# Performance work log

Hardware: AMD Instinct MI355X
Metric: run time of the kernel (lower is better)

The kernel has to match this reference:

```python
import jax, jax.numpy as jnp
import numpy as np

N = 50000
T = 6
E = 800000
F_IN = 64
HID = 64
HEADS = 4
NEG_SLOPE = 0.2
BN_EPS = 1e-5


def _gat_layer(x, src, dst, W, att_src, att_dst, bias, concat):
    # x: [N, Fin]; W: [Fin, H*C]; att_*: [H, C]; src/dst: [E+N] (self loops appended)
    n = x.shape[0]
    H, C = att_src.shape
    xl = (x @ W).reshape(n, H, C)                     # [N, H, C]
    a_src = jnp.sum(xl * att_src[None], axis=-1)      # [N, H]
    a_dst = jnp.sum(xl * att_dst[None], axis=-1)      # [N, H]
    e = jax.nn.leaky_relu(a_src[src] + a_dst[dst], NEG_SLOPE)  # [E', H]
    # segment softmax over destination nodes (every node has a self loop)
    m = jax.ops.segment_max(e, dst, num_segments=n)
    ex = jnp.exp(e - m[dst])
    s = jax.ops.segment_sum(ex, dst, num_segments=n)
    alpha = ex / (s[dst] + 1e-16)                     # [E', H]
    msg = alpha[:, :, None] * xl[src]                 # [E', H, C]
    out = jax.ops.segment_sum(msg, dst, num_segments=n)  # [N, H, C]
    if concat:
        out = out.reshape(n, H * C)
    else:
        out = out.mean(axis=1)
    return out + bias


def _forward(x_seq, edge_index, W1, as1, ad1, b1, W2, as2, ad2, b2,
             cw1, cb1, g1, be1, cw2, cb2, g2, be2, lw1, lb1, lw2, lb2):
    n = x_seq.shape[1]
    self_loop = jnp.arange(n, dtype=edge_index.dtype)
    src = jnp.concatenate([edge_index[0], self_loop])
    dst = jnp.concatenate([edge_index[1], self_loop])

    def per_t(x):
        h = _gat_layer(x, src, dst, W1, as1, ad1, b1, concat=True)
        h = jax.nn.elu(h)
        h = _gat_layer(h, src, dst, W2, as2, ad2, b2, concat=False)
        h = jax.nn.elu(h)
        return h                                      # [N, HID]

    temporal = jax.vmap(per_t)(x_seq)                 # [T, N, HID]
    temporal = jnp.transpose(temporal, (1, 2, 0))     # [N, HID, T]

    def conv_bn_relu(t, cw, cb, g, be):
        y = jax.lax.conv_general_dilated(
            t, cw, window_strides=(1,), padding=[(1, 1)],
            dimension_numbers=('NCH', 'OIH', 'NCH')) + cb[None, :, None]
        # BatchNorm1d in eval mode, running_mean=0, running_var=1
        y = y * (g / jnp.sqrt(1.0 + BN_EPS))[None, :, None] + be[None, :, None]
        return jax.nn.relu(y)

    t = conv_bn_relu(temporal, cw1, cb1, g1, be1)
    t = conv_bn_relu(t, cw2, cb2, g2, be2)
    pooled = t.mean(axis=-1)                          # adaptive avg pool -> [N, HID]
    h = jax.nn.relu(pooled @ lw1 + lb1)
    logits = h @ lw2 + lb2                            # [N, 1]
    return logits


def setup_inputs() -> dict:
    key = jax.random.key(0)
    ks = jax.random.split(key, 20)
    C1 = HID // HEADS  # 16
    s = 0.1
    return {
        'x_seq': jax.random.normal(ks[0], (T, N, F_IN), jnp.float32),
        'edge_index': jax.random.randint(ks[1], (2, E), 0, N, jnp.int32),
        'W1': jax.random.normal(ks[2], (F_IN, HEADS * C1), jnp.float32) * s,
        'as1': jax.random.normal(ks[3], (HEADS, C1), jnp.float32) * s,
        'ad1': jax.random.normal(ks[4], (HEADS, C1), jnp.float32) * s,
        'b1': jnp.zeros((HEADS * C1,), jnp.float32),
        'W2': jax.random.normal(ks[5], (HID, HEADS * HID), jnp.float32) * s,
        'as2': jax.random.normal(ks[6], (HEADS, HID), jnp.float32) * s,
        'ad2': jax.random.normal(ks[7], (HEADS, HID), jnp.float32) * s,
        'b2': jnp.zeros((HID,), jnp.float32),
        'cw1': jax.random.normal(ks[8], (HID, HID, 3), jnp.float32) * s,
        'cb1': jnp.zeros((HID,), jnp.float32),
        'g1': jnp.ones((HID,), jnp.float32),
        'be1': jnp.zeros((HID,), jnp.float32),
        'cw2': jax.random.normal(ks[9], (HID, HID, 3), jnp.float32) * s,
        'cb2': jnp.zeros((HID,), jnp.float32),
        'g2': jnp.ones((HID,), jnp.float32),
        'be2': jnp.zeros((HID,), jnp.float32),
        'lw1': jax.random.normal(ks[10], (HID, HID // 2), jnp.float32) * s,
        'lb1': jnp.zeros((HID // 2,), jnp.float32),
        'lw2': jax.random.normal(ks[11], (HID // 2, 1), jnp.float32) * s,
        'lb2': jnp.zeros((1,), jnp.float32),
    }


def reference(x_seq, edge_index, W1, as1, ad1, b1, W2, as2, ad2, b2,
              cw1, cb1, g1, be1, cw2, cb2, g2, be2, lw1, lb1, lw2, lb2):
    return _forward(x_seq, edge_index, W1, as1, ad1, b1, W2, as2, ad2, b2,
                    cw1, cb1, g1, be1, cw2, cb2, g2, be2, lw1, lb1, lw2, lb2)
```

## Files before the change

### kernel.cpp

```cpp
#include <hip/hip_runtime.h>
#include <math.h>

#define NN 50000
#define EE 800000
#define TT 6

__device__ __forceinline__ float lrelu(float x){ return x > 0.f ? x : 0.2f*x; }
__device__ __forceinline__ float eluf(float x){ return x > 0.f ? x : expm1f(x); }

__global__ void k_init_counts(int* __restrict__ c){
  int i = blockIdx.x*256 + threadIdx.x;
  if (i < NN) c[i] = 1;
}

__global__ void k_hist(const int* __restrict__ dst, int* __restrict__ c){
  int i = blockIdx.x*256 + threadIdx.x;
  if (i < EE) atomicAdd(&c[dst[i]], 1);
}

__global__ void k_scanA(const int* __restrict__ cnt, int* __restrict__ excl,
                        int* __restrict__ bsum){
  __shared__ int sh[1024];
  int tid = threadIdx.x;
  int i = blockIdx.x*1024 + tid;
  int v = (i < NN) ? cnt[i] : 0;
  int x = v;
  sh[tid] = x; __syncthreads();
  for (int off = 1; off < 1024; off <<= 1){
    int y = (tid >= off) ? sh[tid - off] : 0;
    __syncthreads();
    x += y; sh[tid] = x; __syncthreads();
  }
  if (i < NN) excl[i] = x - v;
  if (tid == 1023) bsum[blockIdx.x] = x;
}

__global__ void k_scanB(int* __restrict__ bsum, int nb){
  if (threadIdx.x == 0){
    int run = 0;
    for (int b = 0; b < nb; ++b){ int t = bsum[b]; bsum[b] = run; run += t; }
  }
}

__global__ void k_scanC(const int* __restrict__ excl, const int* __restrict__ bsum,
                        int* __restrict__ rowptr, int* __restrict__ cursor){
  int i = blockIdx.x*1024 + threadIdx.x;
  if (i < NN){
    int v = excl[i] + bsum[blockIdx.x];
    rowptr[i] = v; cursor[i] = v;
  }
  if (i == 0) rowptr[NN] = EE + NN;
}

__global__ void k_scatter(const int* __restrict__ ei, int* __restrict__ cursor,
                          int* __restrict__ csr){
  int i = blockIdx.x*256 + threadIdx.x;
  if (i < EE){
    int d = ei[EE + i];
    int p = atomicAdd(&cursor[d], 1);
    csr[p] = ei[i];
  } else if (i < EE + NN){
    int v = i - EE;
    int p = atomicAdd(&cursor[v], 1);
    csr[p] = v;
  }
}

__global__ void k_prep(const float* __restrict__ W1, const float* __restrict__ as1,
                       const float* __restrict__ ad1,
                       const float* __restrict__ W2, const float* __restrict__ as2,
                       const float* __restrict__ ad2,
                       const float* __restrict__ cw1, const float* __restrict__ cw2,
                       const float* __restrict__ lw1,
                       float* __restrict__ Was1, float* __restrict__ Wad1,
                       float* __restrict__ Wat2, float* __restrict__ Wb,
                       float4* __restrict__ wq1, float4* __restrict__ wq2,
                       float* __restrict__ lw1t){
  int tid = threadIdx.x;
  int k = tid >> 2, h = tid & 3;
  float s1 = 0.f, d1 = 0.f, s2 = 0.f, d2 = 0.f;
  for (int c = 0; c < 16; ++c){
    float w = W1[k*64 + h*16 + c];
    s1 += w * as1[h*16 + c];
    d1 += w * ad1[h*16 + c];
  }
  for (int c = 0; c < 64; ++c){
    float w = W2[k*256 + h*64 + c];
    s2 += w * as2[h*64 + c];
    d2 += w * ad2[h*64 + c];
  }
  Was1[k*4+h] = s1; Wad1[k*4+h] = d1;
  Wat2[k*8 + h] = s2; Wat2[k*8 + 4 + h] = d2;
  for (int idx = tid; idx < 256*64; idx += 256){
    int kf = idx >> 6, c = idx & 63;
    int hh = kf >> 6, kk = kf & 63;
    Wb[idx] = W2[kk*256 + hh*64 + c];
  }
  for (int idx = tid; idx < 64*64; idx += 256){
    int o = idx >> 6, i = idx & 63;
    wq1[idx] = make_float4(cw1[o*192+i*3], cw1[o*192+i*3+1], cw1[o*192+i*3+2], 0.f);
    wq2[idx] = make_float4(cw2[o*192+i*3], cw2[o*192+i*3+1], cw2[o*192+i*3+2], 0.f);
  }
  for (int idx = tid; idx < 32*64; idx += 256){
    int j = idx >> 6, kk = idx & 63;
    lw1t[idx] = lw1[kk*32 + j];
  }
}

__global__ __launch_bounds__(256) void k_gemm_att1(const float* __restrict__ A,
                            const float* __restrict__ W,
                            const float* __restrict__ Was, const float* __restrict__ Wad,
                            float* __restrict__ Xl, float* __restrict__ a_src,
                            float* __restrict__ a_dst){
  __shared__ float At[64][16];
  int tid = threadIdx.x;
  int r0 = blockIdx.x * 16;
  {
    const float4* A4 = (const float4*)(A + (size_t)r0*64);
    float4 v = A4[tid];
    int r = tid >> 4, k4 = (tid & 15) << 2;
    At[k4+0][r] = v.x; At[k4+1][r] = v.y;
    At[k4+2][r] = v.z; At[k4+3][r] = v.w;
  }
  __syncthreads();
  int col = tid & 63;
  int rbase = (tid >> 6) << 2;
  float acc0=0.f, acc1=0.f, acc2=0.f, acc3=0.f;
  for (int k = 0; k < 64; ++k){
    float w = W[k*64 + col];
    float4 a4 = *(const float4*)&At[k][rbase];
    acc0 += a4.x*w; acc1 += a4.y*w; acc2 += a4.z*w; acc3 += a4.w*w;
  }
  Xl[(size_t)(r0+rbase+0)*64 + col] = acc0;
  Xl[(size_t)(r0+rbase+1)*64 + col] = acc1;
  Xl[(size_t)(r0+rbase+2)*64 + col] = acc2;
  Xl[(size_t)(r0+rbase+3)*64 + col] = acc3;
  if (tid < 128){
    int r = tid >> 3, jx = tid & 7;
    int h = jx & 3;
    const float* Wv = (jx < 4) ? Was : Wad;
    float a = 0.f;
    for (int k = 0; k < 64; ++k) a += At[k][r] * Wv[k*4 + h];
    if (jx < 4) a_src[(r0 + r)*4 + h] = a;
    else        a_dst[(r0 + r)*4 + h] = a;
  }
}

__global__ void k_agg1(const float* __restrict__ xl, const float* __restrict__ a_src,
                       const float* __restrict__ a_dst, const float* __restrict__ b1,
                       const float* __restrict__ Wat2,
                       const int* __restrict__ rowptr, const int* __restrict__ csr,
                       float* __restrict__ h1,
                       float* __restrict__ a_src2, float* __restrict__ a_dst2){
  int lane = threadIdx.x & 63;
  int wid  = threadIdx.x >> 6;
  int n = blockIdx.x*4 + wid;
  int h = lane >> 4;
  float ad = a_dst[n*4 + h];
  int rs = rowptr[n], re = rowptr[n+1];
  float s = 0.f, acc = 0.f;
  int j = rs;
  for (; j + 4 <= re; j += 4){
    int sn0=csr[j], sn1=csr[j+1], sn2=csr[j+2], sn3=csr[j+3];
    float e0=a_src[sn0*4+h], e1=a_src[sn1*4+h], e2=a_src[sn2*4+h], e3=a_src[sn3*4+h];
    float x0=xl[(size_t)sn0*64+lane], x1=xl[(size_t)sn1*64+lane];
    float x2=xl[(size_t)sn2*64+lane], x3=xl[(size_t)sn3*64+lane];
    float p0=__expf(lrelu(e0+ad)), p1=__expf(lrelu(e1+ad));
    float p2=__expf(lrelu(e2+ad)), p3=__expf(lrelu(e3+ad));
    s += p0; acc += p0*x0;
    s += p1; acc += p1*x1;
    s += p2; acc += p2*x2;
    s += p3; acc += p3*x3;
  }
  for (; j < re; ++j){
    int sn = csr[j];
    float p = __expf(lrelu(a_src[sn*4+h] + ad));
    float x = xl[(size_t)sn*64 + lane];
    s += p; acc += p*x;
  }
  float hv = eluf(acc/(s + 1e-16f) + b1[lane]);
  h1[(size_t)n*64 + lane] = hv;
  float4 wA = ((const float4*)Wat2)[lane*2];
  float4 wB = ((const float4*)Wat2)[lane*2 + 1];
  float p[8];
  p[0]=hv*wA.x; p[1]=hv*wA.y; p[2]=hv*wA.z; p[3]=hv*wA.w;
  p[4]=hv*wB.x; p[5]=hv*wB.y; p[6]=hv*wB.z; p[7]=hv*wB.w;
#pragma unroll
  for (int off = 32; off >= 1; off >>= 1){
#pragma unroll
    for (int q = 0; q < 8; ++q) p[q] += __shfl_xor(p[q], off);
  }
  if (lane == 0){
    ((float4*)a_src2)[n] = make_float4(p[0],p[1],p[2],p[3]);
    ((float4*)a_dst2)[n] = make_float4(p[4],p[5],p[6],p[7]);
  }
}

__global__ void k_agg2(const float* __restrict__ h1, const float* __restrict__ a_src,
                       const float* __restrict__ a_dst,
                       const int* __restrict__ rowptr, const int* __restrict__ csr,
                       float* __restrict__ agg){
  int lane = threadIdx.x & 63;
  int wid  = threadIdx.x >> 6;
  int n = blockIdx.x*4 + wid;
  float4 ad = ((const float4*)a_dst)[n];
  int rs = rowptr[n], re = rowptr[n+1];
  float s0=0.f,s1=0.f,s2=0.f,s3=0.f;
  float g0=0.f,g1=0.f,g2=0.f,g3=0.f;
  int j = rs;
  for (; j + 4 <= re; j += 4){
    int sa=csr[j], sb=csr[j+1], sc=csr[j+2], sd=csr[j+3];
    float4 ea = ((const float4*)a_src)[sa];
    float4 eb = ((const float4*)a_src)[sb];
    float4 ec = ((const float4*)a_src)[sc];
    float4 ed = ((const float4*)a_src)[sd];
    float xa = h1[(size_t)sa*64 + lane];
    float xb = h1[(size_t)sb*64 + lane];
    float xc = h1[(size_t)sc*64 + lane];
    float xd = h1[(size_t)sd*64 + lane];
    float pa0=__expf(lrelu(ea.x+ad.x)), pa1=__expf(lrelu(ea.y+ad.y));
    float pa2=__expf(lrelu(ea.z+ad.z)), pa3=__expf(lrelu(ea.w+ad.w));
    float pb0=__expf(lrelu(eb.x+ad.x)), pb1=__expf(lrelu(eb.y+ad.y));
    float pb2=__expf(lrelu(eb.z+ad.z)), pb3=__expf(lrelu(eb.w+ad.w));
    float pc0=__expf(lrelu(ec.x+ad.x)), pc1=__expf(lrelu(ec.y+ad.y));
    float pc2=__expf(lrelu(ec.z+ad.z)), pc3=__expf(lrelu(ec.w+ad.w));
    float pd0=__expf(lrelu(ed.x+ad.x)), pd1=__expf(lrelu(ed.y+ad.y));
    float pd2=__expf(lrelu(ed.z+ad.z)), pd3=__expf(lrelu(ed.w+ad.w));
    s0 += pa0+pb0+pc0+pd0; g0 += pa0*xa + pb0*xb + pc0*xc + pd0*xd;
    s1 += pa1+pb1+pc1+pd1; g1 += pa1*xa + pb1*xb + pc1*xc + pd1*xd;
    s2 += pa2+pb2+pc2+pd2; g2 += pa2*xa + pb2*xb + pc2*xc + pd2*xd;
    s3 += pa3+pb3+pc3+pd3; g3 += pa3*xa + pb3*xb + pc3*xc + pd3*xd;
  }
  for (; j < re; ++j){
    int sn = csr[j];
    float4 ev = ((const float4*)a_src)[sn];
    float x = h1[(size_t)sn*64 + lane];
    float p0=__expf(lrelu(ev.x+ad.x)), p1=__expf(lrelu(ev.y+ad.y));
    float p2=__expf(lrelu(ev.z+ad.z)), p3=__expf(lrelu(ev.w+ad.w));
    s0 += p0; g0 += p0*x;
    s1 += p1; g1 += p1*x;
    s2 += p2; g2 += p2*x;
    s3 += p3; g3 += p3*x;
  }
  size_t base = (size_t)n*256 + lane;
  agg[base      ] = g0/(s0 + 1e-16f);
  agg[base +  64] = g1/(s1 + 1e-16f);
  agg[base + 128] = g2/(s2 + 1e-16f);
  agg[base + 192] = g3/(s3 + 1e-16f);
}

__global__ __launch_bounds__(256) void k_out2(const float* __restrict__ agg,
                                              const float* __restrict__ Wb,
                                              const float* __restrict__ b2,
                                              float* __restrict__ ht){
  __shared__ float AtF[256*20];
  int tid = threadIdx.x;
  int r0 = blockIdx.x * 16;
  const float4* A4 = (const float4*)(agg + (size_t)r0*256);
#pragma unroll
  for (int jj = 0; jj < 4; ++jj){
    int m = tid + 256*jj;
    float4 v = A4[m];
    int row = m >> 6, k0 = (m & 63) << 2;
    AtF[(k0+0)*20 + row] = v.x;
    AtF[(k0+1)*20 + row] = v.y;
    AtF[(k0+2)*20 + row] = v.z;
    AtF[(k0+3)*20 + row] = v.w;
  }
  __syncthreads();
  int col = tid & 63;
  int rbase = (tid >> 6) << 2;
  float acc0=0.f, acc1=0.f, acc2=0.f, acc3=0.f;
  for (int k = 0; k < 256; ++k){
    float w = Wb[(size_t)k*64 + col];
    float4 a4 = *(const float4*)&AtF[k*20 + rbase];
    acc0 += a4.x*w; acc1 += a4.y*w; acc2 += a4.z*w; acc3 += a4.w*w;
  }
  float bb = b2[col];
  ht[(size_t)(r0+rbase+0)*64 + col] = eluf(0.25f*acc0 + bb);
  ht[(size_t)(r0+rbase+1)*64 + col] = eluf(0.25f*acc1 + bb);
  ht[(size_t)(r0+rbase+2)*64 + col] = eluf(0.25f*acc2 + bb);
  ht[(size_t)(r0+rbase+3)*64 + col] = eluf(0.25f*acc3 + bb);
}

__global__ __launch_bounds__(256) void k_xposeQ(const float* __restrict__ htb,
                                                float* __restrict__ Xq){
  __shared__ float T[64][65];
  int tid = threadIdx.x;
  int q = tid >> 6, lane = tid & 63;
  int n0 = blockIdx.x * 64;
  int nw = n0 + lane;
  bool ok = (nw < NN);
  for (int jj = 0; jj < 16; ++jj){
    int ch = q*16 + jj;
    if (ok){
      Xq[((size_t)ch*8 + 0)*NN + nw] = 0.f;
      Xq[((size_t)ch*8 + 7)*NN + nw] = 0.f;
    }
  }
  for (int t = 0; t < 6; ++t){
    for (int jj = 0; jj < 16; ++jj){
      int nn = q*16 + jj;
      int nsrc = n0 + nn; if (nsrc >= NN) nsrc = NN-1;
      T[nn][lane] = htb[((size_t)t*NN + nsrc)*64 + lane];
    }
    __syncthreads();
    if (ok){
      for (int jj = 0; jj < 16; ++jj){
        int ch = q*16 + jj;
        Xq[((size_t)ch*8 + t + 1)*NN + nw] = T[lane][ch];
      }
    }
    __syncthreads();
  }
}

__global__ __launch_bounds__(256) void k_convQ(
    const float* __restrict__ Xq, float* __restrict__ C1,
    const float4* __restrict__ wq1, const float* __restrict__ cb1,
    const float* __restrict__ g1,   const float* __restrict__ be1,
    const float4* __restrict__ wq2, const float* __restrict__ cb2,
    const float* __restrict__ g2,   const float* __restrict__ be2,
    const float* __restrict__ lw1t, const float* __restrict__ lb1,
    const float* __restrict__ lw2,  const float* __restrict__ lb2,
    float* __restrict__ out){
  __shared__ float pool_lds[64][65];
  __shared__ float outp[4][64];
  int lane = threadIdx.x & 63;
  int w = __builtin_amdgcn_readfirstlane(threadIdx.x >> 6);
  int n0 = blockIdx.x * 64;
  int n = n0 + lane;
  int nc = (n < NN) ? n : (NN-1);
  bool ok = (n < NN);

#pragma unroll
  for (int oc = 0; oc < 2; ++oc){
    int ob = w*16 + oc*8;
    float acc[8][6];
#pragma unroll
    for (int o = 0; o < 8; ++o){
      float c = cb1[ob+o];
#pragma unroll
      for (int t = 0; t < 6; ++t) acc[o][t] = c;
    }
    for (int i = 0; i < 64; ++i){
      const float* xp = Xq + (size_t)i*8*NN + nc;
      float x0 = xp[0*NN], x1 = xp[1*NN], x2 = xp[2*NN], x3 = xp[3*NN];
      float x4 = xp[4*NN], x5 = xp[5*NN], x6 = xp[6*NN], x7 = xp[7*NN];
#pragma unroll
      for (int o = 0; o < 8; ++o){
        float4 wv = wq1[(ob+o)*64 + i];
        acc[o][0] += wv.x*x0 + wv.y*x1 + wv.z*x2;
        acc[o][1] += wv.x*x1 + wv.y*x2 + wv.z*x3;
        acc[o][2] += wv.x*x2 + wv.y*x3 + wv.z*x4;
        acc[o][3] += wv.x*x3 + wv.y*x4 + wv.z*x5;
        acc[o][4] += wv.x*x4 + wv.y*x5 + wv.z*x6;
        acc[o][5] += wv.x*x5 + wv.y*x6 + wv.z*x7;
      }
    }
    if (ok){
#pragma unroll
      for (int o = 0; o < 8; ++o){
        float bns = g1[ob+o]*rsqrtf(1.f + 1e-5f), be = be1[ob+o];
        float* cp = C1 + (size_t)(ob+o)*8*NN + n;
        cp[0*NN] = 0.f; cp[7*NN] = 0.f;
#pragma unroll
        for (int t = 0; t < 6; ++t) cp[(t+1)*NN] = fmaxf(acc[o][t]*bns + be, 0.f);
      }
    }
  }
  __syncthreads();
#pragma unroll
  for (int oc = 0; oc < 2; ++oc){
    int ob = w*16 + oc*8;
    float acc[8][6];
#pragma unroll
    for (int o = 0; o < 8; ++o){
      float c = cb2[ob+o];
#pragma unroll
      for (int t = 0; t < 6; ++t) acc[o][t] = c;
    }
    for (int i = 0; i < 64; ++i){
      const float* xp = C1 + (size_t)i*8*NN + nc;
      float x0 = xp[0*NN], x1 = xp[1*NN], x2 = xp[2*NN], x3 = xp[3*NN];
      float x4 = xp[4*NN], x5 = xp[5*NN], x6 = xp[6*NN], x7 = xp[7*NN];
#pragma unroll
      for (int o = 0; o < 8; ++o){
        float4 wv = wq2[(ob+o)*64 + i];
        acc[o][0] += wv.x*x0 + wv.y*x1 + wv.z*x2;
        acc[o][1] += wv.x*x1 + wv.y*x2 + wv.z*x3;
        acc[o][2] += wv.x*x2 + wv.y*x3 + wv.z*x4;
        acc[o][3] += wv.x*x3 + wv.y*x4 + wv.z*x5;
        acc[o][4] += wv.x*x4 + wv.y*x5 + wv.z*x6;
        acc[o][5] += wv.x*x5 + wv.y*x6 + wv.z*x7;
      }
    }
#pragma unroll
    for (int o = 0; o < 8; ++o){
      float bns = g2[ob+o]*rsqrtf(1.f + 1e-5f), be = be2[ob+o];
      float pooled = 0.f;
#pragma unroll
      for (int t = 0; t < 6; ++t) pooled += fmaxf(acc[o][t]*bns + be, 0.f);
      pool_lds[ob+o][lane] = pooled*(1.f/6.f);
    }
  }
  __syncthreads();
  {
    float hacc[8];
#pragma unroll
    for (int jj = 0; jj < 8; ++jj) hacc[jj] = 0.f;
    for (int k = 0; k < 64; ++k){
      float pk = pool_lds[k][lane];
#pragma unroll
      for (int jj = 0; jj < 8; ++jj)
        hacc[jj] += pk * lw1t[(w*8+jj)*64 + k];
    }
    float po = 0.f;
#pragma unroll
    for (int jj = 0; jj < 8; ++jj)
      po += fmaxf(hacc[jj] + lb1[w*8+jj], 0.f) * lw2[w*8+jj];
    outp[w][lane] = po;
  }
  __syncthreads();
  if (w == 0 && ok)
    out[n] = outp[0][lane] + outp[1][lane] + outp[2][lane] + outp[3][lane] + lb2[0];
}

extern "C" void kernel_launch(void* const* d_in, const int* in_sizes, int n_in,
                              void* d_out, int out_size, void* d_ws, size_t ws_size,
                              hipStream_t stream) {
  const float* x_seq = (const float*)d_in[0];
  const int*   ei    = (const int*)  d_in[1];
  const float* W1  = (const float*)d_in[2];
  const float* as1 = (const float*)d_in[3];
  const float* ad1 = (const float*)d_in[4];
  const float* b1  = (const float*)d_in[5];
  const float* W2  = (const float*)d_in[6];
  const float* as2 = (const float*)d_in[7];
  const float* ad2 = (const float*)d_in[8];
  const float* b2  = (const float*)d_in[9];
  const float* cw1 = (const float*)d_in[10];
  const float* cb1 = (const float*)d_in[11];
  const float* g1  = (const float*)d_in[12];
  const float* be1 = (const float*)d_in[13];
  const float* cw2 = (const float*)d_in[14];
  const float* cb2 = (const float*)d_in[15];
  const float* g2  = (const float*)d_in[16];
  const float* be2 = (const float*)d_in[17];
  const float* lw1 = (const float*)d_in[18];
  const float* lb1 = (const float*)d_in[19];
  const float* lw2 = (const float*)d_in[20];
  const float* lb2 = (const float*)d_in[21];
  float* out = (float*)d_out;

  const size_t QSZ = (size_t)64*8*NN*sizeof(float);
  char* wp = (char*)d_ws;
  auto alloc = [&](size_t bytes) -> char* {
    char* p = wp; wp += (bytes + 255) & ~(size_t)255; return p;
  };
  char* region1 = alloc(QSZ);
  float* Was1 = (float*)alloc(256*sizeof(float));
  float* Wad1 = (float*)alloc(256*sizeof(float));
  float* Wat2 = (float*)alloc(64*8*sizeof(float));
  float* Wb   = (float*)alloc(256*64*sizeof(float));
  float4* wq1 = (float4*)alloc(64*64*sizeof(float4));
  float4* wq2 = (float4*)alloc(64*64*sizeof(float4));
  float* lw1t = (float*)alloc(32*64*sizeof(float));
  char* region2 = alloc(QSZ);

  char* sp = region1;
  auto salloc = [&](size_t bytes) -> char* {
    char* p = sp; sp += (bytes + 255) & ~(size_t)255; return p;
  };
  int*   counts = (int*)  salloc(NN*sizeof(int));
  int*   excl   = (int*)  salloc(NN*sizeof(int));
  int*   bsum   = (int*)  salloc(64*sizeof(int));
  int*   rowptr = (int*)  salloc((NN+1)*sizeof(int));
  int*   cursor = (int*)  salloc(NN*sizeof(int));
  int*   csr    = (int*)  salloc((size_t)(EE+NN)*sizeof(int));
  float* a_src1 = (float*)salloc((size_t)NN*4*sizeof(float));
  float* a_dst1 = (float*)salloc((size_t)NN*4*sizeof(float));
  float* a_src2 = (float*)salloc((size_t)NN*4*sizeof(float));
  float* a_dst2 = (float*)salloc((size_t)NN*4*sizeof(float));
  float* h1     = (float*)salloc((size_t)NN*64*sizeof(float));
  float* agg    = (float*)salloc((size_t)NN*256*sizeof(float));
  float* xl1    = agg;
  float* Xq     = (float*)region1;
  float* htb    = (float*)region2;
  float* C1     = (float*)region2;

  const int NBSCAN = (NN + 1023)/1024;
  k_init_counts<<<(NN+255)/256, 256, 0, stream>>>(counts);
  k_hist<<<(EE+255)/256, 256, 0, stream>>>(ei + EE, counts);
  k_scanA<<<NBSCAN, 1024, 0, stream>>>(counts, excl, bsum);
  k_scanB<<<1, 64, 0, stream>>>(bsum, NBSCAN);
  k_scanC<<<NBSCAN, 1024, 0, stream>>>(excl, bsum, rowptr, cursor);
  k_scatter<<<(EE+NN+255)/256, 256, 0, stream>>>(ei, cursor, csr);
  k_prep<<<1, 256, 0, stream>>>(W1, as1, ad1, W2, as2, ad2, cw1, cw2, lw1,
                                Was1, Wad1, Wat2, Wb, wq1, wq2, lw1t);

  for (int t = 0; t < TT; ++t){
    const float* xt = x_seq + (size_t)t*NN*64;
    k_gemm_att1<<<NN/16, 256, 0, stream>>>(xt, W1, Was1, Wad1, xl1, a_src1, a_dst1);
    k_agg1<<<NN/4, 256, 0, stream>>>(xl1, a_src1, a_dst1, b1, Wat2, rowptr, csr,
                                     h1, a_src2, a_dst2);
    k_agg2<<<NN/4, 256, 0, stream>>>(h1, a_src2, a_dst2, rowptr, csr, agg);
    k_out2<<<NN/16, 256, 0, stream>>>(agg, Wb, b2, htb + (size_t)t*NN*64);
  }
  const int NB64 = (NN + 63)/64;
  k_xposeQ<<<NB64, 256, 0, stream>>>(htb, Xq);
  k_convQ<<<NB64, 256, 0, stream>>>(Xq, C1, wq1, cb1, g1, be1, wq2, cb2, g2, be2,
                                    lw1t, lb1, lw2, lb2, out);
}
```

Before: 1.432 ms.

## Write GAT output directly in channel-major layout and split temporal conv kernels

k_out2 now writes its ELU output straight into the channel-time-node layout used by the temporal convolution, with float4 stores over four consecutive nodes. This removes the separate transpose kernel and the htb round trip. The zero-padding slots are dropped, so the boundary taps are handled by trimming terms in the conv loops, and the buffer shrinks from 8 to 6 time slots. The fused conv kernel is split into conv1 and conv2 kernels with 16 output channels per wave, which raises register pressure. The output stores are now strided by channel, which may coalesce less well than the previous row-major writes.

```diff
diff --git a/kernel.cpp b/kernel.cpp
--- a/kernel.cpp
+++ b/kernel.cpp
@@ -252,7 +252,7 @@
 __global__ __launch_bounds__(256) void k_out2(const float* __restrict__ agg,
                                               const float* __restrict__ Wb,
                                               const float* __restrict__ b2,
-                                              float* __restrict__ ht){
+                                              float* __restrict__ Xq, int t){
   __shared__ float AtF[256*20];
   int tid = threadIdx.x;
   int r0 = blockIdx.x * 16;
@@ -277,48 +277,54 @@
     acc0 += a4.x*w; acc1 += a4.y*w; acc2 += a4.z*w; acc3 += a4.w*w;
   }
   float bb = b2[col];
-  ht[(size_t)(r0+rbase+0)*64 + col] = eluf(0.25f*acc0 + bb);
-  ht[(size_t)(r0+rbase+1)*64 + col] = eluf(0.25f*acc1 + bb);
-  ht[(size_t)(r0+rbase+2)*64 + col] = eluf(0.25f*acc2 + bb);
-  ht[(size_t)(r0+rbase+3)*64 + col] = eluf(0.25f*acc3 + bb);
-}
-
-__global__ __launch_bounds__(256) void k_xposeQ(const float* __restrict__ htb,
-                                                float* __restrict__ Xq){
-  __shared__ float T[64][65];
-  int tid = threadIdx.x;
-  int q = tid >> 6, lane = tid & 63;
-  int n0 = blockIdx.x * 64;
-  int nw = n0 + lane;
-  bool ok = (nw < NN);
-  for (int jj = 0; jj < 16; ++jj){
-    int ch = q*16 + jj;
-    if (ok){
-      Xq[((size_t)ch*8 + 0)*NN + nw] = 0.f;
-      Xq[((size_t)ch*8 + 7)*NN + nw] = 0.f;
+  float4 v = make_float4(eluf(0.25f*acc0 + bb), eluf(0.25f*acc1 + bb),
+                         eluf(0.25f*acc2 + bb), eluf(0.25f*acc3 + bb));
+  *(float4*)(Xq + ((size_t)col*6 + t)*NN + (r0 + rbase)) = v;
+}
+
+__global__ __launch_bounds__(256) void k_conv1(const float* __restrict__ Xq,
+    float* __restrict__ C1,
+    const float4* __restrict__ wq1, const float* __restrict__ cb1,
+    const float* __restrict__ g1,   const float* __restrict__ be1){
+  int lane = threadIdx.x & 63;
+  int w = __builtin_amdgcn_readfirstlane(threadIdx.x >> 6);
+  int n = blockIdx.x*64 + lane;
+  int nc = (n < NN) ? n : (NN-1);
+  int ob = w*16;
+  float acc[16][6];
+#pragma unroll
+  for (int o = 0; o < 16; ++o){
+    float c = cb1[ob+o];
+#pragma unroll
+    for (int t = 0; t < 6; ++t) acc[o][t] = c;
+  }
+  for (int i = 0; i < 64; ++i){
+    const float* xp = Xq + (size_t)i*6*NN + nc;
+    float x1 = xp[0], x2 = xp[NN], x3 = xp[2*(size_t)NN];
+    float x4 = xp[3*(size_t)NN], x5 = xp[4*(size_t)NN], x6 = xp[5*(size_t)NN];
+#pragma unroll
+    for (int o = 0; o < 16; ++o){
+      float4 wv = wq1[(ob+o)*64 + i];
+      acc[o][0] += wv.y*x1 + wv.z*x2;
+      acc[o][1] += wv.x*x1 + wv.y*x2 + wv.z*x3;
+      acc[o][2] += wv.x*x2 + wv.y*x3 + wv.z*x4;
+      acc[o][3] += wv.x*x3 + wv.y*x4 + wv.z*x5;
+      acc[o][4] += wv.x*x4 + wv.y*x5 + wv.z*x6;
+      acc[o][5] += wv.x*x5 + wv.y*x6;
     }
   }
-  for (int t = 0; t < 6; ++t){
-    for (int jj = 0; jj < 16; ++jj){
-      int nn = q*16 + jj;
-      int nsrc = n0 + nn; if (nsrc >= NN) nsrc = NN-1;
-      T[nn][lane] = htb[((size_t)t*NN + nsrc)*64 + lane];
+  if (n < NN){
+#pragma unroll
+    for (int o = 0; o < 16; ++o){
+      float bns = g1[ob+o]*rsqrtf(1.f + 1e-5f), be = be1[ob+o];
+      float* cp = C1 + (size_t)(ob+o)*6*NN + n;
+#pragma unroll
+      for (int t = 0; t < 6; ++t) cp[(size_t)t*NN] = fmaxf(acc[o][t]*bns + be, 0.f);
     }
-    __syncthreads();
-    if (ok){
-      for (int jj = 0; jj < 16; ++jj){
-        int ch = q*16 + jj;
-        Xq[((size_t)ch*8 + t + 1)*NN + nw] = T[lane][ch];
-      }
-    }
-    __syncthreads();
-  }
-}
-
-__global__ __launch_bounds__(256) void k_convQ(
-    const float* __restrict__ Xq, float* __restrict__ C1,
-    const float4* __restrict__ wq1, const float* __restrict__ cb1,
-    const float* __restrict__ g1,   const float* __restrict__ be1,
+  }
+}
+
+__global__ __launch_bounds__(256) void k_conv2(const float* __restrict__ C1,
     const float4* __restrict__ wq2, const float* __restrict__ cb2,
     const float* __restrict__ g2,   const float* __restrict__ be2,
     const float* __restrict__ lw1t, const float* __restrict__ lb1,
@@ -328,81 +334,38 @@
   __shared__ float outp[4][64];
   int lane = threadIdx.x & 63;
   int w = __builtin_amdgcn_readfirstlane(threadIdx.x >> 6);
-  int n0 = blockIdx.x * 64;
-  int n = n0 + lane;
+  int n = blockIdx.x*64 + lane;
   int nc = (n < NN) ? n : (NN-1);
-  bool ok = (n < NN);
-
-#pragma unroll
-  for (int oc = 0; oc < 2; ++oc){
-    int ob = w*16 + oc*8;
-    float acc[8][6];
-#pragma unroll
-    for (int o = 0; o < 8; ++o){
-      float c = cb1[ob+o];
-#pragma unroll
-      for (int t = 0; t < 6; ++t) acc[o][t] = c;
+  int ob = w*16;
+  float acc[16][6];
+#pragma unroll
+  for (int o = 0; o < 16; ++o){
+    float c = cb2[ob+o];
+#pragma unroll
+    for (int t = 0; t < 6; ++t) acc[o][t] = c;
+  }
+  for (int i = 0; i < 64; ++i){
+    const float* xp = C1 + (size_t)i*6*NN + nc;
+    float x1 = xp[0], x2 = xp[NN], x3 = xp[2*(size_t)NN];
+    float x4 = xp[3*(size_t)NN], x5 = xp[4*(size_t)NN], x6 = xp[5*(size_t)NN];
+#pragma unroll
+    for (int o = 0; o < 16; ++o){
+      float4 wv = wq2[(ob+o)*64 + i];
+      acc[o][0] += wv.y*x1 + wv.z*x2;
+      acc[o][1] += wv.x*x1 + wv.y*x2 + wv.z*x3;
+      acc[o][2] += wv.x*x2 + wv.y*x3 + wv.z*x4;
+      acc[o][3] += wv.x*x3 + wv.y*x4 + wv.z*x5;
+      acc[o][4] += wv.x*x4 + wv.y*x5 + wv.z*x6;
+      acc[o][5] += wv.x*x5 + wv.y*x6;
     }
-    for (int i = 0; i < 64; ++i){
-      const float* xp = Xq + (size_t)i*8*NN + nc;
-      float x0 = xp[0*NN], x1 = xp[1*NN], x2 = xp[2*NN], x3 = xp[3*NN];
-      float x4 = xp[4*NN], x5 = xp[5*NN], x6 = xp[6*NN], x7 = xp[7*NN];
-#pragma unroll
-      for (int o = 0; o < 8; ++o){
-        float4 wv = wq1[(ob+o)*64 + i];
-        acc[o][0] += wv.x*x0 + wv.y*x1 + wv.z*x2;
-        acc[o][1] += wv.x*x1 + wv.y*x2 + wv.z*x3;
-        acc[o][2] += wv.x*x2 + wv.y*x3 + wv.z*x4;
-        acc[o][3] += wv.x*x3 + wv.y*x4 + wv.z*x5;
-        acc[o][4] += wv.x*x4 + wv.y*x5 + wv.z*x6;
-        acc[o][5] += wv.x*x5 + wv.y*x6 + wv.z*x7;
-      }
-    }
-    if (ok){
-#pragma unroll
-      for (int o = 0; o < 8; ++o){
-        float bns = g1[ob+o]*rsqrtf(1.f + 1e-5f), be = be1[ob+o];
-        float* cp = C1 + (size_t)(ob+o)*8*NN + n;
-        cp[0*NN] = 0.f; cp[7*NN] = 0.f;
-#pragma unroll
-        for (int t = 0; t < 6; ++t) cp[(t+1)*NN] = fmaxf(acc[o][t]*bns + be, 0.f);
-      }
-    }
-  }
-  __syncthreads();
-#pragma unroll
-  for (int oc = 0; oc < 2; ++oc){
-    int ob = w*16 + oc*8;
-    float acc[8][6];
-#pragma unroll
-    for (int o = 0; o < 8; ++o){
-      float c = cb2[ob+o];
-#pragma unroll
-      for (int t = 0; t < 6; ++t) acc[o][t] = c;
-    }
-    for (int i = 0; i < 64; ++i){
-      const float* xp = C1 + (size_t)i*8*NN + nc;
-      float x0 = xp[0*NN], x1 = xp[1*NN], x2 = xp[2*NN], x3 = xp[3*NN];
-      float x4 = xp[4*NN], x5 = xp[5*NN], x6 = xp[6*NN], x7 = xp[7*NN];
-#pragma unroll
-      for (int o = 0; o < 8; ++o){
-        float4 wv = wq2[(ob+o)*64 + i];
-        acc[o][0] += wv.x*x0 + wv.y*x1 + wv.z*x2;
-        acc[o][1] += wv.x*x1 + wv.y*x2 + wv.z*x3;
-        acc[o][2] += wv.x*x2 + wv.y*x3 + wv.z*x4;
-        acc[o][3] += wv.x*x3 + wv.y*x4 + wv.z*x5;
-        acc[o][4] += wv.x*x4 + wv.y*x5 + wv.z*x6;
-        acc[o][5] += wv.x*x5 + wv.y*x6 + wv.z*x7;
-      }
-    }
-#pragma unroll
-    for (int o = 0; o < 8; ++o){
-      float bns = g2[ob+o]*rsqrtf(1.f + 1e-5f), be = be2[ob+o];
-      float pooled = 0.f;
-#pragma unroll
-      for (int t = 0; t < 6; ++t) pooled += fmaxf(acc[o][t]*bns + be, 0.f);
-      pool_lds[ob+o][lane] = pooled*(1.f/6.f);
-    }
+  }
+#pragma unroll
+  for (int o = 0; o < 16; ++o){
+    float bns = g2[ob+o]*rsqrtf(1.f + 1e-5f), be = be2[ob+o];
+    float pooled = 0.f;
+#pragma unroll
+    for (int t = 0; t < 6; ++t) pooled += fmaxf(acc[o][t]*bns + be, 0.f);
+    pool_lds[ob+o][lane] = pooled*(1.f/6.f);
   }
   __syncthreads();
   {
@@ -422,7 +385,7 @@
     outp[w][lane] = po;
   }
   __syncthreads();
-  if (w == 0 && ok)
+  if (w == 0 && n < NN)
     out[n] = outp[0][lane] + outp[1][lane] + outp[2][lane] + outp[3][lane] + lb2[0];
 }
 
@@ -453,12 +416,13 @@
   const float* lb2 = (const float*)d_in[21];
   float* out = (float*)d_out;
 
-  const size_t QSZ = (size_t)64*8*NN*sizeof(float);
+  const size_t QSZ = (size_t)64*6*NN*sizeof(float);
   char* wp = (char*)d_ws;
   auto alloc = [&](size_t bytes) -> char* {
     char* p = wp; wp += (bytes + 255) & ~(size_t)255; return p;
   };
   char* region1 = alloc(QSZ);
+  float* Xq = (float*)alloc(QSZ);
   float* Was1 = (float*)alloc(256*sizeof(float));
   float* Wad1 = (float*)alloc(256*sizeof(float));
   float* Wat2 = (float*)alloc(64*8*sizeof(float));
@@ -466,7 +430,6 @@
   float4* wq1 = (float4*)alloc(64*64*sizeof(float4));
   float4* wq2 = (float4*)alloc(64*64*sizeof(float4));
   float* lw1t = (float*)alloc(32*64*sizeof(float));
-  char* region2 = alloc(QSZ);
 
   char* sp = region1;
   auto salloc = [&](size_t bytes) -> char* {
@@ -485,9 +448,7 @@
   float* h1     = (float*)salloc((size_t)NN*64*sizeof(float));
   float* agg    = (float*)salloc((size_t)NN*256*sizeof(float));
   float* xl1    = agg;
-  float* Xq     = (float*)region1;
-  float* htb    = (float*)region2;
-  float* C1     = (float*)region2;
+  float* C1     = (float*)region1;
 
   const int NBSCAN = (NN + 1023)/1024;
   k_init_counts<<<(NN+255)/256, 256, 0, stream>>>(counts);
@@ -505,10 +466,10 @@
     k_agg1<<<NN/4, 256, 0, stream>>>(xl1, a_src1, a_dst1, b1, Wat2, rowptr, csr,
                                      h1, a_src2, a_dst2);
     k_agg2<<<NN/4, 256, 0, stream>>>(h1, a_src2, a_dst2, rowptr, csr, agg);
-    k_out2<<<NN/16, 256, 0, stream>>>(agg, Wb, b2, htb + (size_t)t*NN*64);
+    k_out2<<<NN/16, 256, 0, stream>>>(agg, Wb, b2, Xq, t);
   }
   const int NB64 = (NN + 63)/64;
-  k_xposeQ<<<NB64, 256, 0, stream>>>(htb, Xq);
-  k_convQ<<<NB64, 256, 0, stream>>>(Xq, C1, wq1, cb1, g1, be1, wq2, cb2, g2, be2,
+  k_conv1<<<NB64, 256, 0, stream>>>(Xq, C1, wq1, cb1, g1, be1);
+  k_conv2<<<NB64, 256, 0, stream>>>(C1, wq2, cb2, g2, be2,
                                     lw1t, lb1, lw2, lb2, out);
 }
```

Result: no change. 1.450 ms, median of 2 (+1.3%).
